# Performance work log

Hardware: AMD Instinct MI355X
Metric: run time of the kernel (lower is better)

## Reference

```python
import jax, jax.numpy as jnp
import numpy as np

N_NODES = 50000
HIDDEN = 128
IN_DIM = 128
N_EDGES = 1600000


def gcn_conv(x, W, b, src, dst, deg_isqrt, n_nodes):
    # x: [N, Fin], W: [Fin, Fout]. src/dst include self-loops.
    h = x @ W  # [N, Fout]
    norm = deg_isqrt[src] * deg_isqrt[dst]  # [E+N]
    msgs = h[src] * norm[:, None]  # [E+N, Fout]
    agg = jax.ops.segment_sum(msgs, dst, num_segments=n_nodes)
    return agg + b


def setup_inputs() -> dict:
    key = jax.random.key(0)
    ks = jax.random.split(key, 8)
    x = jax.random.normal(ks[0], (N_NODES, IN_DIM), dtype=jnp.float32)
    edge_index = jax.random.randint(ks[1], (2, N_EDGES), 0, N_NODES, dtype=jnp.int64 if jax.config.jax_enable_x64 else jnp.int32)
    s1 = 1.0 / np.sqrt(IN_DIM)
    s2 = 1.0 / np.sqrt(HIDDEN)
    W1 = jax.random.uniform(ks[2], (IN_DIM, HIDDEN), jnp.float32, -s1, s1)
    b1 = jnp.zeros((HIDDEN,), jnp.float32)
    W2 = jax.random.uniform(ks[3], (HIDDEN, HIDDEN), jnp.float32, -s2, s2)
    b2 = jnp.zeros((HIDDEN,), jnp.float32)
    Wc = jax.random.uniform(ks[4], (HIDDEN, 1), jnp.float32, -s2, s2)
    bc = jnp.zeros((1,), jnp.float32)
    return {"x": x, "edge_index": edge_index, "W1": W1, "b1": b1,
            "W2": W2, "b2": b2, "Wc": Wc, "bc": bc}


def reference(x, edge_index, W1, b1, W2, b2, Wc, bc):
    n = x.shape[0]
    # add self-loops (PyG GCNConv default)
    loop = jnp.arange(n, dtype=edge_index.dtype)
    src = jnp.concatenate([edge_index[0], loop])
    dst = jnp.concatenate([edge_index[1], loop])
    # symmetric normalization: deg over augmented dst, edge weight 1
    deg = jax.ops.segment_sum(jnp.ones_like(dst, dtype=x.dtype), dst, num_segments=n)
    deg_isqrt = jnp.where(deg > 0, jax.lax.rsqrt(deg), 0.0)
    h = jax.nn.relu(gcn_conv(x, W1, b1, src, dst, deg_isqrt, n))
    h = jax.nn.relu(gcn_conv(h, W2, b2, src, dst, deg_isqrt, n))
    return (h @ Wc + bc).squeeze(-1)  # [N]
```

## Files before the change

### kernel.cpp

```cpp
#include <hip/hip_runtime.h>
#include <hip/hip_fp16.h>
#include <cstdint>


#define EPBH 8192
#define DCAP 9216

__global__ __launch_bounds__(256) void bucket_hist(const int* __restrict__ dst,
                                                   int* __restrict__ hist,
                                                   int ne, int nb, int nbuck) {
  __shared__ int lh[256];
  lh[threadIdx.x] = 0;
  __syncthreads();
  int base = blockIdx.x * EPBH;
#pragma unroll
  for (int j = 0; j < 32; ++j) {
    int e = base + j * 256 + threadIdx.x;
    if (e < ne) {
      int d = __builtin_nontemporal_load(&dst[e]);
      atomicAdd(&lh[d >> 8], 1);
    }
  }
  __syncthreads();
  if (threadIdx.x < nbuck)
    hist[(size_t)threadIdx.x * nb + blockIdx.x] = lh[threadIdx.x];
}

__global__ void scan_block(const int* __restrict__ in, int* __restrict__ part,
                           int* __restrict__ bsum, int n) {
  __shared__ int s[1024];
  int i = blockIdx.x * 1024 + threadIdx.x;
  int v = (i < n) ? in[i] : 0;
  s[threadIdx.x] = v;
  __syncthreads();
  for (int off = 1; off < 1024; off <<= 1) {
    int t = (threadIdx.x >= (unsigned)off) ? s[threadIdx.x - off] : 0;
    __syncthreads();
    s[threadIdx.x] += t;
    __syncthreads();
  }
  if (i < n) part[i] = s[threadIdx.x] - v;
  if (threadIdx.x == 1023) bsum[blockIdx.x] = s[1023];
}

__global__ void scan_partials(int* __restrict__ bsum, int nb) {
  __shared__ int s[256];
  int v = (threadIdx.x < (unsigned)nb) ? bsum[threadIdx.x] : 0;
  s[threadIdx.x] = v;
  __syncthreads();
  for (int off = 1; off < 256; off <<= 1) {
    int t = (threadIdx.x >= (unsigned)off) ? s[threadIdx.x - off] : 0;
    __syncthreads();
    s[threadIdx.x] += t;
    __syncthreads();
  }
  if (threadIdx.x < (unsigned)nb) bsum[threadIdx.x] = s[threadIdx.x] - v;
}


__global__ __launch_bounds__(256) void bucket_scatter(const int* __restrict__ src,
                                                      const int* __restrict__ dst,
                                                      const int* __restrict__ part,
                                                      const int* __restrict__ bsum,
                                                      uint32_t* __restrict__ ebuf,
                                                      int ne, int nb, int nbuck) {
  __shared__ int cur[256];
  if (threadIdx.x < nbuck) {
    int idx = threadIdx.x * nb + blockIdx.x;
    cur[threadIdx.x] = part[idx] + bsum[idx >> 10];
  }
  __syncthreads();
  int base = blockIdx.x * EPBH;
#pragma unroll
  for (int j = 0; j < 32; ++j) {
    int e = base + j * 256 + threadIdx.x;
    if (e < ne) {
      int s = __builtin_nontemporal_load(&src[e]);
      int d = __builtin_nontemporal_load(&dst[e]);
      int pos = atomicAdd(&cur[d >> 8], 1);
      ebuf[pos] = ((uint32_t)s << 8) | (uint32_t)(d & 255);
    }
  }
}

__global__ __launch_bounds__(256) void bucket_csr(const uint32_t* __restrict__ ebuf,
                                                  const int* __restrict__ part,
                                                  const int* __restrict__ bsum,
                                                  int* __restrict__ row_ptr,
                                                  float* __restrict__ dinv,
                                                  int* __restrict__ col,
                                                  int ne, int nb, int nbuck, int n) {
  __shared__ int lcnt[256];
  __shared__ int lofs[256];
  __shared__ int cur[256];
  __shared__ uint32_t sbuf[DCAP];
  int b = blockIdx.x;
  int i0 = b * nb;
  int start = part[i0] + bsum[i0 >> 10];
  int end = ne;
  if (b + 1 < nbuck) {
    int i1 = (b + 1) * nb;
    end = part[i1] + bsum[i1 >> 10];
  }
  lcnt[threadIdx.x] = 0;
  __syncthreads();
  for (int k = start + threadIdx.x; k < end; k += 256) {
    uint32_t ed = ebuf[k];
    int rel = k - start;
    if (rel < DCAP) sbuf[rel] = ed;
    atomicAdd(&lcnt[ed & 255u], 1);
  }
  __syncthreads();
  int v = lcnt[threadIdx.x];
  lofs[threadIdx.x] = v;
  __syncthreads();
  for (int off = 1; off < 256; off <<= 1) {
    int t = (threadIdx.x >= (unsigned)off) ? lofs[threadIdx.x - off] : 0;
    __syncthreads();
    lofs[threadIdx.x] += t;
    __syncthreads();
  }
  int excl = lofs[threadIdx.x] - v;
  int node = b * 256 + threadIdx.x;
  if (node < n) {
    row_ptr[node] = start + excl;
    dinv[node] = rsqrtf((float)(v + 1));
  }
  cur[threadIdx.x] = start + excl;
  __syncthreads();
  for (int k = start + threadIdx.x; k < end; k += 256) {
    int rel = k - start;
    uint32_t ed = (rel < DCAP) ? sbuf[rel] : ebuf[k];
    int pos = atomicAdd(&cur[ed & 255u], 1);
    col[pos] = (int)(ed >> 8);
  }
  if (b == nbuck - 1 && threadIdx.x == 0) row_ptr[n] = ne;
}


typedef _Float16 half_t;
typedef __attribute__((ext_vector_type(8))) _Float16 f16x8;
typedef __attribute__((ext_vector_type(4))) float f32x4;

#define LDP 136

__device__ __forceinline__ void gemm_core(half_t (*As)[LDP], half_t (*Bs)[LDP],
                                          const float* __restrict__ dinv,
                                          __half* __restrict__ out,
                                          int row0, int nrows, int tid) {
  int wv = tid >> 6;
  int lane = tid & 63;
  int m = lane & 15;
  int kg = lane >> 4;

  f32x4 acc[8];
#pragma unroll
  for (int ct = 0; ct < 8; ++ct) acc[ct] = (f32x4){0.f, 0.f, 0.f, 0.f};

#pragma unroll
  for (int ks = 0; ks < 4; ++ks) {
    f16x8 a = *(const f16x8*)&As[wv * 16 + m][ks * 32 + kg * 8];
#pragma unroll
    for (int ct = 0; ct < 8; ++ct) {
      f16x8 b = *(const f16x8*)&Bs[ct * 16 + m][ks * 32 + kg * 8];
      acc[ct] = __builtin_amdgcn_mfma_f32_16x16x32_f16(a, b, acc[ct], 0, 0, 0);
    }
  }

  int orow = row0 + wv * 16 + kg * 4;
  float d0 = (orow + 0 < nrows) ? dinv[orow + 0] : 0.f;
  float d1 = (orow + 1 < nrows) ? dinv[orow + 1] : 0.f;
  float d2 = (orow + 2 < nrows) ? dinv[orow + 2] : 0.f;
  float d3 = (orow + 3 < nrows) ? dinv[orow + 3] : 0.f;
#pragma unroll
  for (int ct = 0; ct < 8; ++ct) {
    int ocol = ct * 16 + m;
    if (orow + 0 < nrows) out[(size_t)(orow + 0) * 128 + ocol] = __float2half_rn(acc[ct][0] * d0);
    if (orow + 1 < nrows) out[(size_t)(orow + 1) * 128 + ocol] = __float2half_rn(acc[ct][1] * d1);
    if (orow + 2 < nrows) out[(size_t)(orow + 2) * 128 + ocol] = __float2half_rn(acc[ct][2] * d2);
    if (orow + 3 < nrows) out[(size_t)(orow + 3) * 128 + ocol] = __float2half_rn(acc[ct][3] * d3);
  }
}

__device__ __forceinline__ void stage_W(half_t (*Bs)[LDP], const float* __restrict__ W, int tid) {
#pragma unroll
  for (int it = 0; it < 16; ++it) {
    int idx = it * 256 + tid;
    int k = idx >> 5;
    int f4 = (idx & 31) * 4;
    float4 w = *(const float4*)&W[(size_t)k * 128 + f4];
    Bs[f4 + 0][k] = (half_t)w.x;
    Bs[f4 + 1][k] = (half_t)w.y;
    Bs[f4 + 2][k] = (half_t)w.z;
    Bs[f4 + 3][k] = (half_t)w.w;
  }
}

__global__ __launch_bounds__(256) void gemm_mfma_f32in(const float* __restrict__ in,
                                                       const float* __restrict__ W,
                                                       const float* __restrict__ dinv,
                                                       __half* __restrict__ out, int nrows) {
  __shared__ half_t As[64][LDP];
  __shared__ half_t Bs[128][LDP];
  int tid = threadIdx.x;
  int row0 = blockIdx.x * 64;
  stage_W(Bs, W, tid);
#pragma unroll
  for (int it = 0; it < 8; ++it) {
    int idx = it * 256 + tid;
    int r = idx >> 5;
    int k4 = (idx & 31) * 4;
    int grow = row0 + r;
    float4 v = make_float4(0.f, 0.f, 0.f, 0.f);
    if (grow < nrows) v = *(const float4*)&in[(size_t)grow * 128 + k4];
    As[r][k4 + 0] = (half_t)v.x;
    As[r][k4 + 1] = (half_t)v.y;
    As[r][k4 + 2] = (half_t)v.z;
    As[r][k4 + 3] = (half_t)v.w;
  }
  __syncthreads();
  gemm_core(As, Bs, dinv, out, row0, nrows, tid);
}

__global__ __launch_bounds__(256) void gemm_mfma_f16in(const __half* __restrict__ in,
                                                       const float* __restrict__ W,
                                                       const float* __restrict__ dinv,
                                                       __half* __restrict__ out, int nrows) {
  __shared__ half_t As[64][LDP];
  __shared__ half_t Bs[128][LDP];
  int tid = threadIdx.x;
  int row0 = blockIdx.x * 64;
  stage_W(Bs, W, tid);
#pragma unroll
  for (int it = 0; it < 4; ++it) {
    int idx = it * 256 + tid;
    int r = idx >> 4;
    int k8 = (idx & 15) * 8;
    int grow = row0 + r;
    uint4 v = make_uint4(0u, 0u, 0u, 0u);
    if (grow < nrows) v = *(const uint4*)&in[(size_t)grow * 128 + k8];
    *(uint4*)&As[r][k8] = v;
  }
  __syncthreads();
  gemm_core(As, Bs, dinv, out, row0, nrows, tid);
}


__device__ inline float4 h4_to_f4(uint2 u) {
  __half2 a = *(__half2*)&u.x;
  __half2 b = *(__half2*)&u.y;
  float2 fa = __half22float2(a);
  float2 fb = __half22float2(b);
  return make_float4(fa.x, fa.y, fb.x, fb.y);
}


__global__ __launch_bounds__(256) void aggregate_h(const __half* __restrict__ hsh,
                                                   const int* __restrict__ row_ptr,
                                                   const int* __restrict__ col,
                                                   const float* __restrict__ dinv,
                                                   const float* __restrict__ bias,
                                                   __half* __restrict__ out, int n) {
  int node = (blockIdx.x * blockDim.x + threadIdx.x) >> 6;
  if (node >= n) return;
  int lane = threadIdx.x & 63;
  int half_ = lane >> 5;
  int f4 = lane & 31;
  const uint2* rows = (const uint2*)hsh;

  int start = row_ptr[node];
  int end = row_ptr[node + 1];

  float4 acc = make_float4(0.f, 0.f, 0.f, 0.f);
  if (half_ == 0) acc = h4_to_f4(rows[(size_t)node * 32 + f4]);

  int e = start + half_;
  for (; e + 14 < end; e += 16) {
    uint2 u[8];
#pragma unroll
    for (int j = 0; j < 8; ++j) u[j] = rows[(size_t)col[e + 2 * j] * 32 + f4];
#pragma unroll
    for (int j = 0; j < 8; ++j) {
      float4 v = h4_to_f4(u[j]);
      acc.x += v.x; acc.y += v.y; acc.z += v.z; acc.w += v.w;
    }
  }
  for (; e < end; e += 2) {
    float4 v = h4_to_f4(rows[(size_t)col[e] * 32 + f4]);
    acc.x += v.x; acc.y += v.y; acc.z += v.z; acc.w += v.w;
  }

  acc.x += __shfl_xor(acc.x, 32);
  acc.y += __shfl_xor(acc.y, 32);
  acc.z += __shfl_xor(acc.z, 32);
  acc.w += __shfl_xor(acc.w, 32);

  if (half_ == 0) {
    float d = dinv[node];
    float4 b = ((const float4*)bias)[f4];
    __half2 h01 = __floats2half2_rn(fmaxf(acc.x * d + b.x, 0.f), fmaxf(acc.y * d + b.y, 0.f));
    __half2 h23 = __floats2half2_rn(fmaxf(acc.z * d + b.z, 0.f), fmaxf(acc.w * d + b.w, 0.f));
    uint2 o = make_uint2(*(uint*)&h01, *(uint*)&h23);
    ((uint2*)out)[(size_t)node * 32 + f4] = o;
  }
}


__global__ __launch_bounds__(256) void aggregate_dot_h(const __half* __restrict__ hsh,
                                                       const int* __restrict__ row_ptr,
                                                       const int* __restrict__ col,
                                                       const float* __restrict__ dinv,
                                                       const float* __restrict__ bias,
                                                       const float* __restrict__ Wc,
                                                       const float* __restrict__ bc,
                                                       float* __restrict__ out, int n) {
  int node = (blockIdx.x * blockDim.x + threadIdx.x) >> 6;
  if (node >= n) return;
  int lane = threadIdx.x & 63;
  int half_ = lane >> 5;
  int f4 = lane & 31;
  const uint2* rows = (const uint2*)hsh;

  int start = row_ptr[node];
  int end = row_ptr[node + 1];

  float4 acc = make_float4(0.f, 0.f, 0.f, 0.f);
  if (half_ == 0) acc = h4_to_f4(rows[(size_t)node * 32 + f4]);

  int e = start + half_;
  for (; e + 14 < end; e += 16) {
    uint2 u[8];
#pragma unroll
    for (int j = 0; j < 8; ++j) u[j] = rows[(size_t)col[e + 2 * j] * 32 + f4];
#pragma unroll
    for (int j = 0; j < 8; ++j) {
      float4 v = h4_to_f4(u[j]);
      acc.x += v.x; acc.y += v.y; acc.z += v.z; acc.w += v.w;
    }
  }
  for (; e < end; e += 2) {
    float4 v = h4_to_f4(rows[(size_t)col[e] * 32 + f4]);
    acc.x += v.x; acc.y += v.y; acc.z += v.z; acc.w += v.w;
  }

  acc.x += __shfl_xor(acc.x, 32);
  acc.y += __shfl_xor(acc.y, 32);
  acc.z += __shfl_xor(acc.z, 32);
  acc.w += __shfl_xor(acc.w, 32);

  float d = dinv[node];
  float4 b = ((const float4*)bias)[f4];
  float4 w = ((const float4*)Wc)[f4];
  float s = fmaxf(acc.x * d + b.x, 0.f) * w.x
          + fmaxf(acc.y * d + b.y, 0.f) * w.y
          + fmaxf(acc.z * d + b.z, 0.f) * w.z
          + fmaxf(acc.w * d + b.w, 0.f) * w.w;
#pragma unroll
  for (int off = 16; off; off >>= 1) s += __shfl_xor(s, off);
  if (lane == 0) out[node] = s + bc[0];
}


extern "C" void kernel_launch(void* const* d_in, const int* in_sizes, int n_in,
                              void* d_out, int out_size, void* d_ws, size_t ws_size,
                              hipStream_t stream) {
  const float* x  = (const float*)d_in[0];
  const int* ei   = (const int*)d_in[1];
  const float* W1 = (const float*)d_in[2];
  const float* b1 = (const float*)d_in[3];
  const float* W2 = (const float*)d_in[4];
  const float* b2 = (const float*)d_in[5];
  const float* Wc = (const float*)d_in[6];
  const float* bc = (const float*)d_in[7];
  float* out = (float*)d_out;

  int n  = in_sizes[0] / 128;
  int ne = in_sizes[1] / 2;
  const int* src = ei;
  const int* dst = ei + ne;

  int NBb = (ne + EPBH - 1) / EPBH;
  int NBUCK = (n + 255) >> 8;
  int HN = NBUCK * NBb;

  char* p = (char*)d_ws;
  auto alloc = [&](size_t bytes) {
    char* r = p;
    p += (bytes + 255) & ~(size_t)255;
    return r;
  };
  int*    hist    = (int*)alloc((size_t)HN * 4);
  int*    part    = (int*)alloc((size_t)HN * 4);
  int*    bsum    = (int*)alloc(256 * 4);
  int*    row_ptr = (int*)alloc((size_t)(n + 1) * 4);
  float*  dinv    = (float*)alloc((size_t)n * 4);
  int*    col     = (int*)alloc((size_t)ne * 4);
  __half* hsh     = (__half*)alloc((size_t)n * 128 * 2);
  __half* h1      = (__half*)alloc((size_t)n * 128 * 2);
  uint32_t* ebuf  = (uint32_t*)alloc((size_t)ne * 4);

  bucket_hist<<<NBb, 256, 0, stream>>>(dst, hist, ne, NBb, NBUCK);
  int nsb = (HN + 1023) / 1024;
  scan_block<<<nsb, 1024, 0, stream>>>(hist, part, bsum, HN);
  scan_partials<<<1, 256, 0, stream>>>(bsum, nsb);
  bucket_scatter<<<NBb, 256, 0, stream>>>(src, dst, part, bsum, ebuf, ne, NBb, NBUCK);
  bucket_csr<<<NBUCK, 256, 0, stream>>>(ebuf, part, bsum, row_ptr, dinv, col, ne, NBb, NBUCK, n);

  int gemm_blocks = (n + 63) / 64;
  int agg_blocks = (n + 3) / 4;

  gemm_mfma_f32in<<<gemm_blocks, 256, 0, stream>>>(x, W1, dinv, hsh, n);
  aggregate_h<<<agg_blocks, 256, 0, stream>>>(hsh, row_ptr, col, dinv, b1, h1, n);
  gemm_mfma_f16in<<<gemm_blocks, 256, 0, stream>>>(h1, W2, dinv, hsh, n);
  aggregate_dot_h<<<agg_blocks, 256, 0, stream>>>(hsh, row_ptr, col, dinv, b2, Wc, bc, out, n);
}
```

Before: 229.3 us.

## Fuse CSR construction kernels into one cooperative kernel with grid syncs

Replaces the five CSR-building launches (histogram, two-level scan, scatter, per-bucket sort) with a single cooperative kernel that uses grid.sync between phases. The scan is restructured as a per-bucket scan over source blocks plus a single-block scan of bucket totals. The aim is to remove launch gaps and per-kernel tail overhead. In exchange the grid is limited to co-resident blocks and pays grid-wide barrier costs; the per-bucket scan assumes at most 256 edge blocks.

```diff
diff --git a/kernel.cpp b/kernel.cpp
--- a/kernel.cpp
+++ b/kernel.cpp
@@ -1,140 +1,135 @@
 #include <hip/hip_runtime.h>
+#include <hip/hip_cooperative_groups.h>
 #include <hip/hip_fp16.h>
 #include <cstdint>
 
+namespace cg = cooperative_groups;
+
 
 #define EPBH 8192
 #define DCAP 9216
 
-__global__ __launch_bounds__(256) void bucket_hist(const int* __restrict__ dst,
-                                                   int* __restrict__ hist,
-                                                   int ne, int nb, int nbuck) {
+__global__ __launch_bounds__(256) void build_csr_coop(
+    const int* __restrict__ src, const int* __restrict__ dst,
+    int* __restrict__ hist,
+    int* __restrict__ bt,
+    int* __restrict__ bko,
+    int* __restrict__ row_ptr, float* __restrict__ dinv,
+    int* __restrict__ col, uint32_t* __restrict__ ebuf,
+    int ne, int nb, int nbuck, int n) {
+  cg::grid_group grid = cg::this_grid();
   __shared__ int lh[256];
-  lh[threadIdx.x] = 0;
-  __syncthreads();
-  int base = blockIdx.x * EPBH;
-#pragma unroll
-  for (int j = 0; j < 32; ++j) {
-    int e = base + j * 256 + threadIdx.x;
-    if (e < ne) {
-      int d = __builtin_nontemporal_load(&dst[e]);
-      atomicAdd(&lh[d >> 8], 1);
-    }
-  }
-  __syncthreads();
-  if (threadIdx.x < nbuck)
-    hist[(size_t)threadIdx.x * nb + blockIdx.x] = lh[threadIdx.x];
-}
-
-__global__ void scan_block(const int* __restrict__ in, int* __restrict__ part,
-                           int* __restrict__ bsum, int n) {
-  __shared__ int s[1024];
-  int i = blockIdx.x * 1024 + threadIdx.x;
-  int v = (i < n) ? in[i] : 0;
-  s[threadIdx.x] = v;
-  __syncthreads();
-  for (int off = 1; off < 1024; off <<= 1) {
-    int t = (threadIdx.x >= (unsigned)off) ? s[threadIdx.x - off] : 0;
-    __syncthreads();
-    s[threadIdx.x] += t;
-    __syncthreads();
-  }
-  if (i < n) part[i] = s[threadIdx.x] - v;
-  if (threadIdx.x == 1023) bsum[blockIdx.x] = s[1023];
-}
-
-__global__ void scan_partials(int* __restrict__ bsum, int nb) {
-  __shared__ int s[256];
-  int v = (threadIdx.x < (unsigned)nb) ? bsum[threadIdx.x] : 0;
-  s[threadIdx.x] = v;
-  __syncthreads();
-  for (int off = 1; off < 256; off <<= 1) {
-    int t = (threadIdx.x >= (unsigned)off) ? s[threadIdx.x - off] : 0;
-    __syncthreads();
-    s[threadIdx.x] += t;
-    __syncthreads();
-  }
-  if (threadIdx.x < (unsigned)nb) bsum[threadIdx.x] = s[threadIdx.x] - v;
-}
-
-
-__global__ __launch_bounds__(256) void bucket_scatter(const int* __restrict__ src,
-                                                      const int* __restrict__ dst,
-                                                      const int* __restrict__ part,
-                                                      const int* __restrict__ bsum,
-                                                      uint32_t* __restrict__ ebuf,
-                                                      int ne, int nb, int nbuck) {
-  __shared__ int cur[256];
-  if (threadIdx.x < nbuck) {
-    int idx = threadIdx.x * nb + blockIdx.x;
-    cur[threadIdx.x] = part[idx] + bsum[idx >> 10];
-  }
-  __syncthreads();
-  int base = blockIdx.x * EPBH;
-#pragma unroll
-  for (int j = 0; j < 32; ++j) {
-    int e = base + j * 256 + threadIdx.x;
-    if (e < ne) {
-      int s = __builtin_nontemporal_load(&src[e]);
-      int d = __builtin_nontemporal_load(&dst[e]);
-      int pos = atomicAdd(&cur[d >> 8], 1);
-      ebuf[pos] = ((uint32_t)s << 8) | (uint32_t)(d & 255);
-    }
-  }
-}
-
-__global__ __launch_bounds__(256) void bucket_csr(const uint32_t* __restrict__ ebuf,
-                                                  const int* __restrict__ part,
-                                                  const int* __restrict__ bsum,
-                                                  int* __restrict__ row_ptr,
-                                                  float* __restrict__ dinv,
-                                                  int* __restrict__ col,
-                                                  int ne, int nb, int nbuck, int n) {
-  __shared__ int lcnt[256];
-  __shared__ int lofs[256];
+  __shared__ int ls[256];
   __shared__ int cur[256];
   __shared__ uint32_t sbuf[DCAP];
   int b = blockIdx.x;
-  int i0 = b * nb;
-  int start = part[i0] + bsum[i0 >> 10];
-  int end = ne;
-  if (b + 1 < nbuck) {
-    int i1 = (b + 1) * nb;
-    end = part[i1] + bsum[i1 >> 10];
-  }
-  lcnt[threadIdx.x] = 0;
-  __syncthreads();
-  for (int k = start + threadIdx.x; k < end; k += 256) {
-    uint32_t ed = ebuf[k];
-    int rel = k - start;
-    if (rel < DCAP) sbuf[rel] = ed;
-    atomicAdd(&lcnt[ed & 255u], 1);
-  }
-  __syncthreads();
-  int v = lcnt[threadIdx.x];
-  lofs[threadIdx.x] = v;
-  __syncthreads();
-  for (int off = 1; off < 256; off <<= 1) {
-    int t = (threadIdx.x >= (unsigned)off) ? lofs[threadIdx.x - off] : 0;
-    __syncthreads();
-    lofs[threadIdx.x] += t;
-    __syncthreads();
-  }
-  int excl = lofs[threadIdx.x] - v;
-  int node = b * 256 + threadIdx.x;
-  if (node < n) {
-    row_ptr[node] = start + excl;
-    dinv[node] = rsqrtf((float)(v + 1));
-  }
-  cur[threadIdx.x] = start + excl;
-  __syncthreads();
-  for (int k = start + threadIdx.x; k < end; k += 256) {
-    int rel = k - start;
-    uint32_t ed = (rel < DCAP) ? sbuf[rel] : ebuf[k];
-    int pos = atomicAdd(&cur[ed & 255u], 1);
-    col[pos] = (int)(ed >> 8);
-  }
-  if (b == nbuck - 1 && threadIdx.x == 0) row_ptr[n] = ne;
+  int t = threadIdx.x;
+
+  if (b < nb) {
+    lh[t] = 0;
+    __syncthreads();
+    int base = b * EPBH;
+#pragma unroll
+    for (int j = 0; j < 32; ++j) {
+      int e = base + j * 256 + t;
+      if (e < ne) {
+        int d = __builtin_nontemporal_load(&dst[e]);
+        atomicAdd(&lh[d >> 8], 1);
+      }
+    }
+    __syncthreads();
+    if (t < nbuck) hist[(size_t)t * nb + b] = lh[t];
+  }
+  __threadfence();
+  grid.sync();
+
+  if (b < nbuck) {
+    int v = (t < nb) ? hist[(size_t)b * nb + t] : 0;
+    ls[t] = v;
+    __syncthreads();
+    for (int off = 1; off < 256; off <<= 1) {
+      int x = (t >= off) ? ls[t - off] : 0;
+      __syncthreads();
+      ls[t] += x;
+      __syncthreads();
+    }
+    if (t < nb) hist[(size_t)b * nb + t] = ls[t] - v;
+    if (t == 255) bt[b] = ls[255];
+  }
+  __threadfence();
+  grid.sync();
+
+  if (b == 0) {
+    int v = (t < nbuck) ? bt[t] : 0;
+    ls[t] = v;
+    __syncthreads();
+    for (int off = 1; off < 256; off <<= 1) {
+      int x = (t >= off) ? ls[t - off] : 0;
+      __syncthreads();
+      ls[t] += x;
+      __syncthreads();
+    }
+    if (t < nbuck) bko[t] = ls[t] - v;
+    if (t == 0) bko[nbuck] = ne;
+  }
+  __threadfence();
+  grid.sync();
+
+  if (b < nb) {
+    if (t < nbuck) cur[t] = hist[(size_t)t * nb + b] + bko[t];
+    __syncthreads();
+    int base = b * EPBH;
+#pragma unroll
+    for (int j = 0; j < 32; ++j) {
+      int e = base + j * 256 + t;
+      if (e < ne) {
+        int s = __builtin_nontemporal_load(&src[e]);
+        int d = __builtin_nontemporal_load(&dst[e]);
+        int pos = atomicAdd(&cur[d >> 8], 1);
+        ebuf[pos] = ((uint32_t)s << 8) | (uint32_t)(d & 255);
+      }
+    }
+  }
+  __threadfence();
+  grid.sync();
+
+  if (b < nbuck) {
+    int start = bko[b];
+    int end = bko[b + 1];
+    lh[t] = 0;
+    __syncthreads();
+    for (int k = start + t; k < end; k += 256) {
+      uint32_t ed = ebuf[k];
+      int rel = k - start;
+      if (rel < DCAP) sbuf[rel] = ed;
+      atomicAdd(&lh[ed & 255u], 1);
+    }
+    __syncthreads();
+    int v = lh[t];
+    ls[t] = v;
+    __syncthreads();
+    for (int off = 1; off < 256; off <<= 1) {
+      int x = (t >= off) ? ls[t - off] : 0;
+      __syncthreads();
+      ls[t] += x;
+      __syncthreads();
+    }
+    int excl = ls[t] - v;
+    int node = b * 256 + t;
+    if (node < n) {
+      row_ptr[node] = start + excl;
+      dinv[node] = rsqrtf((float)(v + 1));
+    }
+    cur[t] = start + excl;
+    __syncthreads();
+    for (int k = start + t; k < end; k += 256) {
+      int rel = k - start;
+      uint32_t ed = (rel < DCAP) ? sbuf[rel] : ebuf[k];
+      int pos = atomicAdd(&cur[ed & 255u], 1);
+      col[pos] = (int)(ed >> 8);
+    }
+    if (b == 0 && t == 0) row_ptr[n] = ne;
+  }
 }
 
 
@@ -390,8 +385,8 @@
     return r;
   };
   int*    hist    = (int*)alloc((size_t)HN * 4);
-  int*    part    = (int*)alloc((size_t)HN * 4);
-  int*    bsum    = (int*)alloc(256 * 4);
+  int*    bt      = (int*)alloc(256 * 4);
+  int*    bko     = (int*)alloc(260 * 4);
   int*    row_ptr = (int*)alloc((size_t)(n + 1) * 4);
   float*  dinv    = (float*)alloc((size_t)n * 4);
   int*    col     = (int*)alloc((size_t)ne * 4);
@@ -399,12 +394,12 @@
   __half* h1      = (__half*)alloc((size_t)n * 128 * 2);
   uint32_t* ebuf  = (uint32_t*)alloc((size_t)ne * 4);
 
-  bucket_hist<<<NBb, 256, 0, stream>>>(dst, hist, ne, NBb, NBUCK);
-  int nsb = (HN + 1023) / 1024;
-  scan_block<<<nsb, 1024, 0, stream>>>(hist, part, bsum, HN);
-  scan_partials<<<1, 256, 0, stream>>>(bsum, nsb);
-  bucket_scatter<<<NBb, 256, 0, stream>>>(src, dst, part, bsum, ebuf, ne, NBb, NBUCK);
-  bucket_csr<<<NBUCK, 256, 0, stream>>>(ebuf, part, bsum, row_ptr, dinv, col, ne, NBb, NBUCK, n);
+  int gblocks = NBb > NBUCK ? NBb : NBUCK;
+  void* cargs[] = {(void*)&src, (void*)&dst, (void*)&hist, (void*)&bt, (void*)&bko,
+                   (void*)&row_ptr, (void*)&dinv, (void*)&col, (void*)&ebuf,
+                   (void*)&ne, (void*)&NBb, (void*)&NBUCK, (void*)&n};
+  hipLaunchCooperativeKernel((const void*)build_csr_coop, dim3(gblocks), dim3(256),
+                             cargs, 0, stream);
 
   int gemm_blocks = (n + 63) / 64;
   int agg_blocks = (n + 3) / 4;
```

After: 416.7 us. 1.82x slower.
